# Kernel optimization log

Hardware: AMD Instinct MI355X
Metric: run time of the kernel (lower is better)

## Reference

```python
import jax, jax.numpy as jnp
import numpy as np

B, S, D, H = 4, 2048, 1024, 16
HD = D // H


def setup_inputs() -> dict:
    key = jax.random.key(0)
    ks = jax.random.split(key, 5)
    scale = 1.0 / np.sqrt(D)
    return {
        "x": jax.random.normal(ks[0], (B, S, D), dtype=jnp.float32),
        "W_q": jax.random.normal(ks[1], (D, D), dtype=jnp.float32) * scale,
        "W_k": jax.random.normal(ks[2], (D, D), dtype=jnp.float32) * scale,
        "W_v": jax.random.normal(ks[3], (D, D), dtype=jnp.float32) * scale,
        "W_o": jax.random.normal(ks[4], (D, D), dtype=jnp.float32) * scale,
    }


def reference(x, W_q, W_k, W_v, W_o):
    b, s, d = x.shape
    # fused QKV projections; reshape to per-head layout [b, s, H, HD]
    q = (x @ W_q).reshape(b, s, H, HD)
    k = (x @ W_k).reshape(b, s, H, HD)
    v = (x @ W_v).reshape(b, s, H, HD)
    # scaled dot-product scores [b, H, s, s]
    scores = jnp.einsum("bqhd,bkhd->bhqk", q, k) / jnp.sqrt(jnp.asarray(HD, x.dtype))
    # causal mask: disallow attending to future positions (j > i)
    causal = jnp.tril(jnp.ones((s, s), dtype=bool))
    scores = jnp.where(causal[None, None], scores, jnp.finfo(x.dtype).min)
    attn = jax.nn.softmax(scores, axis=-1)
    # attention output back to [b, s, d], then output projection (W_o applied as x @ W_o.T)
    out = jnp.einsum("bhqk,bkhd->bqhd", attn, v).reshape(b, s, d)
    return out @ W_o.T
```

## Files before the change

kernel.cpp:

```cpp
#include <hip/hip_runtime.h>
#include <hip/hip_bf16.h>
#include <stdint.h>

#define B_  4
#define S_  2048
#define D_  1024
#define H_  16
#define HD_ 64
#define M_  (B_*S_)

typedef __bf16 bf16_t;
typedef __bf16 bf16x8 __attribute__((ext_vector_type(8)));
typedef __bf16 bf16x4 __attribute__((ext_vector_type(4)));
typedef __bf16 bf16x2 __attribute__((ext_vector_type(2)));
typedef float  f32x4  __attribute__((ext_vector_type(4)));
typedef unsigned int uint2v __attribute__((ext_vector_type(2)));

#define EXP2(x) __builtin_amdgcn_exp2f(x)

__global__ void cvt_f32_to_bf16(const float* __restrict__ src, bf16_t* __restrict__ dst, int n) {
  int stride = gridDim.x * blockDim.x * 4;
  for (int i = (blockIdx.x * blockDim.x + threadIdx.x) * 4; i < n; i += stride) {
    float4 v = *(const float4*)(src + i);
    bf16x4 o = { (bf16_t)v.x, (bf16_t)v.y, (bf16_t)v.z, (bf16_t)v.w };
    *(bf16x4*)(dst + i) = o;
  }
}

__global__ void cvt_transpose_w(const float* __restrict__ wq, const float* __restrict__ wk,
                                const float* __restrict__ wv, const float* __restrict__ wof,
                                bf16_t* __restrict__ dst, bf16_t* __restrict__ wob) {
  __shared__ float t[32][33];
  int w = blockIdx.z;
  int c0 = blockIdx.x * 32, r0 = blockIdx.y * 32;
  int tx = threadIdx.x, ty = threadIdx.y;
  if (w == 3) {
#pragma unroll
    for (int i = 0; i < 4; i++)
      wob[(size_t)(r0 + ty + i * 8) * D_ + c0 + tx] =
          (bf16_t)wof[(size_t)(r0 + ty + i * 8) * D_ + c0 + tx];
    return;
  }
  const float* src = (w == 0) ? wq : (w == 1) ? wk : wv;
#pragma unroll
  for (int i = 0; i < 4; i++)
    t[ty + i * 8][tx] = src[(size_t)(r0 + ty + i * 8) * D_ + c0 + tx];
  __syncthreads();
#pragma unroll
  for (int i = 0; i < 4; i++)
    dst[(size_t)(w * D_ + c0 + ty + i * 8) * D_ + r0 + tx] = (bf16_t)t[tx][ty + i * 8];
}

template <typename OutT>
__global__ void gemm_nt(const bf16_t* __restrict__ A, const bf16_t* __restrict__ Bt,
                        OutT* __restrict__ C, int Mt, int N, int K) {
  __shared__ bf16_t As[128 * 32];
  __shared__ bf16_t Bs[128 * 32];
  const int bn = blockIdx.x, bm = blockIdx.y;
  const int tid = threadIdx.x;
  const int wv = tid >> 6, lane = tid & 63;
  const int wr = wv >> 1, wc = wv & 1;
  const int g = lane >> 4, r16 = lane & 15;
  const int m0 = bm * 128, n0 = bn * 128;

  f32x4 acc[4][4] = {};

  for (int kt = 0; kt < K; kt += 32) {
#pragma unroll
    for (int c = 0; c < 2; c++) {
      int ch = wv * 2 + c;
      int o = ch * 1024 + lane * 16;
      int row = o >> 6, colb = o & 63;
      const bf16_t* gA = A + (size_t)(m0 + row) * K + kt + (colb >> 1);
      __builtin_amdgcn_global_load_lds((const __attribute__((address_space(1))) void*)gA,
          (__attribute__((address_space(3))) void*)((char*)As + ch * 1024), 16, 0, 0);
    }
#pragma unroll
    for (int c = 0; c < 2; c++) {
      int ch = wv * 2 + c;
      int o = ch * 1024 + lane * 16;
      int row = o >> 6, colb = o & 63;
      const bf16_t* gB = Bt + (size_t)(n0 + row) * K + kt + (colb >> 1);
      __builtin_amdgcn_global_load_lds((const __attribute__((address_space(1))) void*)gB,
          (__attribute__((address_space(3))) void*)((char*)Bs + ch * 1024), 16, 0, 0);
    }
    __syncthreads();

    bf16x8 af[4], bfv[4];
#pragma unroll
    for (int i = 0; i < 4; i++) {
      int row = wr * 64 + i * 16 + r16;
      af[i] = *(const bf16x8*)(As + row * 32 + g * 8);
    }
#pragma unroll
    for (int j = 0; j < 4; j++) {
      int row = wc * 64 + j * 16 + r16;
      bfv[j] = *(const bf16x8*)(Bs + row * 32 + g * 8);
    }
#pragma unroll
    for (int i = 0; i < 4; i++)
#pragma unroll
      for (int j = 0; j < 4; j++)
        acc[i][j] = __builtin_amdgcn_mfma_f32_16x16x32_bf16(af[i], bfv[j], acc[i][j], 0, 0, 0);
    __syncthreads();
  }

#pragma unroll
  for (int i = 0; i < 4; i++)
#pragma unroll
    for (int j = 0; j < 4; j++)
#pragma unroll
      for (int rr = 0; rr < 4; rr++) {
        int grow = m0 + wr * 64 + i * 16 + g * 4 + rr;
        int gcol = n0 + wc * 64 + j * 16 + r16;
        C[(size_t)grow * N + gcol] = (OutT)acc[i][j][rr];
      }
}

__global__ __launch_bounds__(256, 3) void attn_kernel(const bf16_t* __restrict__ QKV,
                                                      bf16_t* __restrict__ AO) {
  const int bh = blockIdx.x;
  const int y = (int)blockIdx.y;
  const int jj = y >> 2, gq = y & 3;
  const int qt = (jj == 0) ? (15 - gq) : (jj == 1) ? (8 + gq) : (jj == 2) ? (7 - gq) : gq;
  const int b = bh >> 4, h = bh & 15;
  const int tid = threadIdx.x, wv = tid >> 6, lane = tid & 63;
  const int g = lane >> 4, r16 = lane & 15;
  const bool b4 = (g & 1) != 0;

  __shared__ bf16_t Ks[2][64 * 64];
  __shared__ bf16_t Vt[2][64 * 64];

  const size_t rowbase = (size_t)b * S_;
  const bf16_t* Qg = QKV + (rowbase + qt * 128) * 3072 + h * HD_;
  const bf16_t* Kg = QKV + rowbase * 3072 + 1024 + h * HD_;
  const bf16_t* Vg = QKV + rowbase * 3072 + 2048 + h * HD_;

  bf16x8 qf[2][2];
#pragma unroll
  for (int rg = 0; rg < 2; rg++) {
    int row = wv * 32 + rg * 16 + r16;
    const bf16_t* p = Qg + (size_t)row * 3072;
    qf[rg][0] = *(const bf16x8*)(p + g * 8);
    qf[rg][1] = *(const bf16x8*)(p + 32 + g * 8);
  }

  f32x4 o_acc[2][4] = {};
  float mrow[2] = {-1e30f, -1e30f};
  float lrow[2] = {0.f, 0.f};
  const float cs = 0.125f * 1.44269504088896f;

  int base_row[2];
  base_row[0] = qt * 128 + wv * 32;
  base_row[1] = base_row[0] + 16;

  const int kp0 = tid >> 4, dq = tid & 15;
  bf16x4 va0, vb0, va1, vb1;

  auto issueK = [&](int t, int buf) {
    const int kv0 = t * 64;
#pragma unroll
    for (int c = 0; c < 2; c++) {
      int chunkid = wv * 2 + c;
      int o = chunkid * 1024 + lane * 16;
      int row = o >> 7;
      int ch = (o >> 4) & 7;
      const bf16_t* src = Kg + (size_t)(kv0 + row) * 3072 + ((ch ^ (row & 7)) * 8);
      __builtin_amdgcn_global_load_lds((const __attribute__((address_space(1))) void*)src,
          (__attribute__((address_space(3))) void*)((char*)(&Ks[buf][0]) + chunkid * 1024), 16, 0, 0);
    }
  };
  auto loadV = [&](int t) {
    const int kv0 = t * 64;
    const bf16_t* p0 = Vg + (size_t)(kv0 + kp0 * 2) * 3072 + dq * 4;
    va0 = *(const bf16x4*)p0;
    vb0 = *(const bf16x4*)(p0 + 3072);
    const bf16_t* p1 = Vg + (size_t)(kv0 + (16 + kp0) * 2) * 3072 + dq * 4;
    va1 = *(const bf16x4*)p1;
    vb1 = *(const bf16x4*)(p1 + 3072);
  };
  auto writeV = [&](int buf) {
#pragma unroll
    for (int j = 0; j < 4; j++) {
      int d = dq * 4 + j;
      int sz = (((d & 7) ^ (d >> 3)) << 2);
      bf16x2 q0 = { va0[j], vb0[j] };
      *(bf16x2*)(&Vt[buf][d * 64 + (kp0 ^ sz) * 2]) = q0;
      bf16x2 q1 = { va1[j], vb1[j] };
      *(bf16x2*)(&Vt[buf][d * 64 + ((16 + kp0) ^ sz) * 2]) = q1;
    }
  };

  issueK(0, 0);
  loadV(0);

  const int ntiles = 2 * qt + 2;
  for (int t = 0; t < ntiles; t++) {
    const int cur = t & 1;
    const int kv0 = t * 64;

    asm volatile("s_waitcnt vmcnt(0)" ::: "memory");
    writeV(cur);
    __syncthreads();
    if (t + 1 < ntiles) { issueK(t + 1, cur ^ 1); loadV(t + 1); }

    bool skip[2], needmask[2];
#pragma unroll
    for (int rg = 0; rg < 2; rg++) {
      skip[rg] = kv0 > base_row[rg] + 15;
      needmask[rg] = (kv0 + 63) > base_row[rg];
    }

    f32x4 st[2][4];
    __builtin_amdgcn_s_setprio(1);
#pragma unroll
    for (int sub = 0; sub < 4; sub++) {
      int krow = sub * 16 + r16;
      bf16x8 k0 = *(const bf16x8*)((char*)(&Ks[cur][0]) + krow * 128 + ((g ^ (krow & 7)) * 16));
      bf16x8 k1 = *(const bf16x8*)((char*)(&Ks[cur][0]) + krow * 128 + (((4 + g) ^ (krow & 7)) * 16));
#pragma unroll
      for (int rg = 0; rg < 2; rg++) {
        if (skip[rg]) continue;
        if (kv0 + sub * 16 > base_row[rg] + 15) {
          f32x4 ninf = { -1e30f, -1e30f, -1e30f, -1e30f };
          st[rg][sub] = ninf;
          continue;
        }
        f32x4 z = {};
        z = __builtin_amdgcn_mfma_f32_16x16x32_bf16(k0, qf[rg][0], z, 0, 0, 0);
        z = __builtin_amdgcn_mfma_f32_16x16x32_bf16(k1, qf[rg][1], z, 0, 0, 0);
        st[rg][sub] = z;
      }
    }
    __builtin_amdgcn_s_setprio(0);

    bf16x8 pf[2][2];
#pragma unroll
    for (int rg = 0; rg < 2; rg++) {
      if (skip[rg]) continue;
      const int qrow = base_row[rg] + r16;
      if (needmask[rg]) {
#pragma unroll
        for (int sub = 0; sub < 4; sub++)
#pragma unroll
          for (int rr = 0; rr < 4; rr++)
            if (kv0 + sub * 16 + g * 4 + rr > qrow) st[rg][sub][rr] = -1e30f;
      }
      float m0v = fmaxf(fmaxf(st[rg][0][0], st[rg][0][1]), st[rg][0][2]);
      float m1v = fmaxf(fmaxf(st[rg][0][3], st[rg][1][0]), st[rg][1][1]);
      float m2v = fmaxf(fmaxf(st[rg][1][2], st[rg][1][3]), st[rg][2][0]);
      float m3v = fmaxf(fmaxf(st[rg][2][1], st[rg][2][2]), st[rg][2][3]);
      float m4v = fmaxf(fmaxf(st[rg][3][0], st[rg][3][1]), st[rg][3][2]);
      float v = fmaxf(fmaxf(fmaxf(m0v, m1v), fmaxf(m2v, m3v)), fmaxf(m4v, st[rg][3][3]));
      v = fmaxf(v, __shfl_xor(v, 16));
      v = fmaxf(v, __shfl_xor(v, 32));
      if (!__all((v - mrow[rg]) * cs <= 8.0f)) {
        float mnew = fmaxf(mrow[rg], v);
        float scf = EXP2((mrow[rg] - mnew) * cs);
        mrow[rg] = mnew;
        lrow[rg] *= scf;
#pragma unroll
        for (int c = 0; c < 4; c++)
#pragma unroll
          for (int rr = 0; rr < 4; rr++) o_acc[rg][c][rr] *= scf;
      }
      const float mc = mrow[rg] * cs;
      float lsum = 0.f;
      unsigned int W[4][2];
#pragma unroll
      for (int sub = 0; sub < 4; sub++)
#pragma unroll
        for (int rrp = 0; rrp < 2; rrp++) {
          float p0 = EXP2(__builtin_fmaf(st[rg][sub][2 * rrp], cs, -mc));
          float p1 = EXP2(__builtin_fmaf(st[rg][sub][2 * rrp + 1], cs, -mc));
          lsum += p0 + p1;
          bf16x2 pp = { (bf16_t)p0, (bf16_t)p1 };
          W[sub][rrp] = *(unsigned int*)&pp;
        }
      lrow[rg] += lsum;
      unsigned int pfw[2][4];
#pragma unroll
      for (int k2 = 0; k2 < 2; k2++)
#pragma unroll
        for (int rrp = 0; rrp < 2; rrp++) {
          uint2v xy = __builtin_amdgcn_permlane32_swap(W[2 * k2][rrp], W[2 * k2 + 1][rrp],
                                                       false, false);
          unsigned X = xy[0], Y = xy[1];
          unsigned send2 = b4 ? X : Y;
          unsigned keep2 = b4 ? Y : X;
          unsigned got = (unsigned)__shfl_xor((int)send2, 16);
          pfw[k2][rrp]     = b4 ? got : keep2;
          pfw[k2][2 + rrp] = b4 ? keep2 : got;
        }
#pragma unroll
      for (int kh = 0; kh < 2; kh++) {
        union { unsigned int u[4]; bf16x8 v8; } U;
        U.u[0] = pfw[kh][0]; U.u[1] = pfw[kh][1];
        U.u[2] = pfw[kh][2]; U.u[3] = pfw[kh][3];
        pf[rg][kh] = U.v8;
      }
    }

    __builtin_amdgcn_s_setprio(1);
#pragma unroll
    for (int kh = 0; kh < 2; kh++) {
#pragma unroll
      for (int c = 0; c < 4; c++) {
        int d = c * 16 + r16;
        int wstart = (kh * 16 + g * 4) ^ (((d & 7) ^ (d >> 3)) << 2);
        bf16x8 vf = *(const bf16x8*)(&Vt[cur][d * 64 + wstart * 2]);
#pragma unroll
        for (int rg = 0; rg < 2; rg++) {
          if (skip[rg]) continue;
          o_acc[rg][c] = __builtin_amdgcn_mfma_f32_16x16x32_bf16(vf, pf[rg][kh], o_acc[rg][c], 0, 0, 0);
        }
      }
    }
    __builtin_amdgcn_s_setprio(0);
  }

#pragma unroll
  for (int rg = 0; rg < 2; rg++) {
    float v = lrow[rg];
    v += __shfl_xor(v, 16);
    v += __shfl_xor(v, 32);
    float linv = 1.0f / v;
    const size_t grow = rowbase + base_row[rg] + r16;
#pragma unroll
    for (int c = 0; c < 4; c++) {
      bf16x4 o = { (bf16_t)(o_acc[rg][c][0] * linv), (bf16_t)(o_acc[rg][c][1] * linv),
                   (bf16_t)(o_acc[rg][c][2] * linv), (bf16_t)(o_acc[rg][c][3] * linv) };
      *(bf16x4*)(&AO[grow * D_ + h * HD_ + c * 16 + g * 4]) = o;
    }
  }
}

extern "C" void kernel_launch(void* const* d_in, const int* in_sizes, int n_in,
                              void* d_out, int out_size, void* d_ws, size_t ws_size,
                              hipStream_t stream) {
  const float* x  = (const float*)d_in[0];
  const float* Wq = (const float*)d_in[1];
  const float* Wk = (const float*)d_in[2];
  const float* Wv = (const float*)d_in[3];
  const float* Wo = (const float*)d_in[4];
  float* out = (float*)d_out;

  char* ws = (char*)d_ws;
  bf16_t* xb   = (bf16_t*)(ws);
  bf16_t* wqkv = (bf16_t*)(ws + 16777216);
  bf16_t* wo   = (bf16_t*)(ws + 16777216 + 6291456);
  bf16_t* qkv  = (bf16_t*)(ws + 25165824);
  bf16_t* ao   = (bf16_t*)(ws + 75497472);

  cvt_f32_to_bf16<<<1024, 256, 0, stream>>>(x, xb, M_ * D_);
  cvt_transpose_w<<<dim3(32, 32, 4), dim3(32, 8), 0, stream>>>(Wq, Wk, Wv, Wo, wqkv, wo);

  gemm_nt<bf16_t><<<dim3(3072 / 128, M_ / 128), 256, 0, stream>>>(xb, wqkv, qkv, M_, 3072, D_);

  attn_kernel<<<dim3(B_ * H_, 16), 256, 0, stream>>>(qkv, ao);

  gemm_nt<float><<<dim3(D_ / 128, M_ / 128), 256, 0, stream>>>(ao, wo, out, M_, D_, D_);
}
```

Measured before the change: 187.8 us.

## Deepen attention K/V prefetch to two tiles ahead with triple-buffered K

The attention loop now prefetches K and V two tiles ahead instead of one. K uses three LDS buffers with a rotating index, and V uses two register sets (even/odd) so loads for tile t+2 can be in flight while tile t computes. A partial vmcnt wait replaces the full drain before each V write, which is meant to hide global memory latency. In exchange it uses more LDS (an extra 8KB K buffer) and more registers, which may reduce occupancy at launch_bounds(256,3). Correctness also depends on the vmcnt(6) count matching the loads still outstanding.

```diff
diff --git a/kernel.cpp b/kernel.cpp
--- a/kernel.cpp
+++ b/kernel.cpp
@@ -128,7 +128,7 @@
   const int g = lane >> 4, r16 = lane & 15;
   const bool b4 = (g & 1) != 0;
 
-  __shared__ bf16_t Ks[2][64 * 64];
+  __shared__ bf16_t Ks[3][64 * 64];
   __shared__ bf16_t Vt[2][64 * 64];
 
   const size_t rowbase = (size_t)b * S_;
@@ -155,7 +155,8 @@
   base_row[1] = base_row[0] + 16;
 
   const int kp0 = tid >> 4, dq = tid & 15;
-  bf16x4 va0, vb0, va1, vb1;
+  bf16x4 e0, e1, e2, e3;
+  bf16x4 o0, o1, o2, o3;
 
   auto issueK = [&](int t, int buf) {
     const int kv0 = t * 64;
@@ -170,40 +171,74 @@
           (__attribute__((address_space(3))) void*)((char*)(&Ks[buf][0]) + chunkid * 1024), 16, 0, 0);
     }
   };
-  auto loadV = [&](int t) {
+  auto loadVE = [&](int t) {
     const int kv0 = t * 64;
     const bf16_t* p0 = Vg + (size_t)(kv0 + kp0 * 2) * 3072 + dq * 4;
-    va0 = *(const bf16x4*)p0;
-    vb0 = *(const bf16x4*)(p0 + 3072);
+    e0 = *(const bf16x4*)p0;
+    e1 = *(const bf16x4*)(p0 + 3072);
     const bf16_t* p1 = Vg + (size_t)(kv0 + (16 + kp0) * 2) * 3072 + dq * 4;
-    va1 = *(const bf16x4*)p1;
-    vb1 = *(const bf16x4*)(p1 + 3072);
+    e2 = *(const bf16x4*)p1;
+    e3 = *(const bf16x4*)(p1 + 3072);
   };
-  auto writeV = [&](int buf) {
+  auto loadVO = [&](int t) {
+    const int kv0 = t * 64;
+    const bf16_t* p0 = Vg + (size_t)(kv0 + kp0 * 2) * 3072 + dq * 4;
+    o0 = *(const bf16x4*)p0;
+    o1 = *(const bf16x4*)(p0 + 3072);
+    const bf16_t* p1 = Vg + (size_t)(kv0 + (16 + kp0) * 2) * 3072 + dq * 4;
+    o2 = *(const bf16x4*)p1;
+    o3 = *(const bf16x4*)(p1 + 3072);
+  };
+  auto writeVE = [&]() {
 #pragma unroll
     for (int j = 0; j < 4; j++) {
       int d = dq * 4 + j;
       int sz = (((d & 7) ^ (d >> 3)) << 2);
-      bf16x2 q0 = { va0[j], vb0[j] };
-      *(bf16x2*)(&Vt[buf][d * 64 + (kp0 ^ sz) * 2]) = q0;
-      bf16x2 q1 = { va1[j], vb1[j] };
-      *(bf16x2*)(&Vt[buf][d * 64 + ((16 + kp0) ^ sz) * 2]) = q1;
+      bf16x2 q0 = { e0[j], e1[j] };
+      *(bf16x2*)(&Vt[0][d * 64 + (kp0 ^ sz) * 2]) = q0;
+      bf16x2 q1 = { e2[j], e3[j] };
+      *(bf16x2*)(&Vt[0][d * 64 + ((16 + kp0) ^ sz) * 2]) = q1;
     }
   };
-
+  auto writeVO = [&]() {
+#pragma unroll
+    for (int j = 0; j < 4; j++) {
+      int d = dq * 4 + j;
+      int sz = (((d & 7) ^ (d >> 3)) << 2);
+      bf16x2 q0 = { o0[j], o1[j] };
+      *(bf16x2*)(&Vt[1][d * 64 + (kp0 ^ sz) * 2]) = q0;
+      bf16x2 q1 = { o2[j], o3[j] };
+      *(bf16x2*)(&Vt[1][d * 64 + ((16 + kp0) ^ sz) * 2]) = q1;
+    }
+  };
+
+  const int ntiles = 2 * qt + 2;
+
+  loadVE(0);
   issueK(0, 0);
-  loadV(0);
-
-  const int ntiles = 2 * qt + 2;
+  __builtin_amdgcn_sched_barrier(0);
+  issueK(1, 1);
+  __builtin_amdgcn_sched_barrier(0);
+  loadVO(1);
+
+  int kb = 0;
   for (int t = 0; t < ntiles; t++) {
-    const int cur = t & 1;
+    const int vcur = t & 1;
+
+    if (t + 1 < ntiles) { asm volatile("s_waitcnt vmcnt(6)" ::: "memory"); }
+    else                { asm volatile("s_waitcnt vmcnt(0)" ::: "memory"); }
+    if (vcur == 0) writeVE(); else writeVO();
+    asm volatile("s_waitcnt lgkmcnt(0)" ::: "memory");
+    __builtin_amdgcn_s_barrier();
+    __builtin_amdgcn_sched_barrier(0);
+    if (t + 2 < ntiles) {
+      int kb2 = kb + 2; if (kb2 >= 3) kb2 -= 3;
+      issueK(t + 2, kb2);
+      __builtin_amdgcn_sched_barrier(0);
+      if (vcur == 0) loadVE(t + 2); else loadVO(t + 2);
+    }
+
     const int kv0 = t * 64;
-
-    asm volatile("s_waitcnt vmcnt(0)" ::: "memory");
-    writeV(cur);
-    __syncthreads();
-    if (t + 1 < ntiles) { issueK(t + 1, cur ^ 1); loadV(t + 1); }
-
     bool skip[2], needmask[2];
 #pragma unroll
     for (int rg = 0; rg < 2; rg++) {
@@ -216,8 +251,8 @@
 #pragma unroll
     for (int sub = 0; sub < 4; sub++) {
       int krow = sub * 16 + r16;
-      bf16x8 k0 = *(const bf16x8*)((char*)(&Ks[cur][0]) + krow * 128 + ((g ^ (krow & 7)) * 16));
-      bf16x8 k1 = *(const bf16x8*)((char*)(&Ks[cur][0]) + krow * 128 + (((4 + g) ^ (krow & 7)) * 16));
+      bf16x8 k0 = *(const bf16x8*)((char*)(&Ks[kb][0]) + krow * 128 + ((g ^ (krow & 7)) * 16));
+      bf16x8 k1 = *(const bf16x8*)((char*)(&Ks[kb][0]) + krow * 128 + (((4 + g) ^ (krow & 7)) * 16));
 #pragma unroll
       for (int rg = 0; rg < 2; rg++) {
         if (skip[rg]) continue;
@@ -308,7 +343,7 @@
       for (int c = 0; c < 4; c++) {
         int d = c * 16 + r16;
         int wstart = (kh * 16 + g * 4) ^ (((d & 7) ^ (d >> 3)) << 2);
-        bf16x8 vf = *(const bf16x8*)(&Vt[cur][d * 64 + wstart * 2]);
+        bf16x8 vf = *(const bf16x8*)(&Vt[vcur][d * 64 + wstart * 2]);
 #pragma unroll
         for (int rg = 0; rg < 2; rg++) {
           if (skip[rg]) continue;
@@ -317,6 +352,8 @@
       }
     }
     __builtin_amdgcn_s_setprio(0);
+
+    kb++; if (kb == 3) kb = 0;
   }
 
 #pragma unroll
```

Measured after the change: 201.2 us. 7.2% more time.
